# Kernel optimization log

Hardware: AMD Instinct MI355X
Metric: run time of the kernel (lower is better)

Reference implementation:

```python
import math
import jax, jax.numpy as jnp
import numpy as np

MIN_SIGMA = 1.0
MAX_SIGMA = 10.0
SIGMA_BINS = 50
TRUNCATE = 5.0
THRESHOLD = 0.001
H = W = 1024


def _make_sigmas():
    # np.linspace(min, max + (max-min)/bins, bins+1)
    return np.linspace(MIN_SIGMA, MAX_SIGMA + (MAX_SIGMA - MIN_SIGMA) / SIGMA_BINS,
                       num=SIGMA_BINS + 1).astype(np.float32)


def _make_pyramid_weight(sigmas):
    max_radius = int(TRUNCATE * float(sigmas.max()) + 0.5)
    size = 2 * max_radius + 1
    weight = np.zeros((len(sigmas), 1, size, size), dtype=np.float32)
    for i, s in enumerate(sigmas):
        r = int(TRUNCATE * float(s) + 0.5)
        ax = np.arange(2 * r + 1, dtype=np.float32)
        g = (1.0 / (s * math.sqrt(2 * math.pi))) * np.exp(-((ax - r) / s) ** 2 / 2)
        k = np.outer(g, g)
        k /= k.sum()
        pad = max_radius - r
        weight[i, 0, pad:pad + 2 * r + 1, pad:pad + 2 * r + 1] = k
    return weight, max_radius


def setup_inputs() -> dict:
    key = jax.random.key(0)
    sigmas_np = _make_sigmas()
    weight_np, _ = _make_pyramid_weight(sigmas_np)
    x = jax.random.normal(key, (1, 1, H, W), dtype=jnp.float32)
    return {
        "input": x,
        "weight": jnp.asarray(weight_np),            # [51, 1, 101, 101]
        "sigmas": jnp.asarray(sigmas_np),            # [51]
        "threshold": jnp.asarray(-THRESHOLD, dtype=jnp.float32),  # nn.Parameter(-threshold)
    }


def reference(input, weight, sigmas, threshold):
    max_radius = (weight.shape[-1] - 1) // 2
    # Gaussian pyramid: [1, 51, H, W], zero 'same' padding
    g = jax.lax.conv_general_dilated(
        input, weight,
        window_strides=(1, 1),
        padding=((max_radius, max_radius), (max_radius, max_radius)),
        dimension_numbers=("NCHW", "OIHW", "NCHW"),
    )[0]                                             # [51, H, W]
    # DoG scaled by sigma: [50, H, W]
    dog = (g[:-1] - g[1:]) * sigmas[:-1, None, None]
    # 3D local max pooling over (scale, y, x), kernel 3, stride 1, pad 1
    pooled = jax.lax.reduce_window(
        dog, -jnp.inf, jax.lax.max,
        window_dimensions=(3, 3, 3),
        window_strides=(1, 1, 1),
        padding=((1, 1), (1, 1), (1, 1)),
    )
    local_maxima = jax.nn.relu(pooled + threshold)
    soft_mask = 1.0 - (local_maxima - (dog + threshold))
    return local_maxima, soft_mask
```

## Files before the change

kernel.cpp:

```cpp
#include <hip/hip_runtime.h>
#include <cmath>

#define NS 51
#define ND 50
#define PLANE 1048576
#define DOG_ELEMS (ND * PLANE)
#define WPSTRIDE 160

__global__ void dog_prep(const float* __restrict__ weight,
                         float* __restrict__ wp,
                         int* __restrict__ rarr, int S) {
    int i = blockIdx.x;
    int t = threadIdx.x;
    int R = (S - 1) >> 1;
    const float* row = weight + ((size_t)i * S + R) * S;
    __shared__ float sr[128];
    __shared__ float ssum;
    __shared__ int spad;
    if (t < S) sr[t] = row[t];
    for (int j = t; j < WPSTRIDE; j += blockDim.x) wp[i * WPSTRIDE + j] = 0.f;
    __syncthreads();
    if (t == 0) {
        float sum = 0.f;
        for (int j = 0; j < S; ++j) sum += sr[j];
        int pad = 0;
        while (pad < R && sr[pad] == 0.f) ++pad;
        ssum = sum; spad = pad;
        rarr[i] = R - pad;
    }
    __syncthreads();
    int pad = spad;
    int r = R - pad;
    float inv = 1.f / ssum;
    for (int j = t; j <= 2 * r; j += blockDim.x)
        wp[i * WPSTRIDE + 17 + j] = sr[pad + j] * inv;
}

__global__ __launch_bounds__(256) void dog_hblur(
        const float* __restrict__ in, float* __restrict__ tmpH,
        const float* __restrict__ wp, const int* __restrict__ rarr) {
    const int lo_t[5] = {0, 17, 28, 37, 44};
    const int hi_t[5] = {17, 28, 37, 44, 51};
    int t = threadIdx.x;
    int grp = t >> 7;
    int tl = t & 127;
    int y = (blockIdx.x << 1) | grp;
    int zc = blockIdx.y;
    __shared__ float srow[2][1284];
    const float* inrow = in + ((size_t)y << 10);
    for (int f = tl; f < 286; f += 128) {
        int xg = (f << 2) - 56;
        float4 v = make_float4(0.f, 0.f, 0.f, 0.f);
        if (xg >= 0 && xg <= 1020) {
            v = *(const float4*)(inrow + xg);
        } else {
            float vv[4];
#pragma unroll
            for (int c = 0; c < 4; ++c) {
                int g = xg + c;
                vv[c] = ((unsigned)g < 1024u) ? inrow[g] : 0.f;
            }
            v = make_float4(vv[0], vv[1], vv[2], vv[3]);
        }
        int fs = f + (f >> 3);
        *(float4*)&srow[grp][fs << 2] = v;
    }
    __syncthreads();
    const float* s = srow[grp];
    for (int i = lo_t[zc]; i < hi_t[zc]; ++i) {
        int r = rarr[i];
        int c0 = 56 - r;
        int d = c0 & 7;
        int c0a = c0 - d;
        const float* __restrict__ w2 = wp + i * WPSTRIDE + 17 - d;
        int mcount = ((2 * r + d + 15) >> 3) << 3;
        float acc[8];
#pragma unroll
        for (int k = 0; k < 8; ++k) acc[k] = 0.f;
        int ft = (c0a >> 2) + (tl << 1);
        for (int m = 0; m < mcount; m += 8) {
            int f  = ft + (m >> 2);
            int fa = f + (f >> 3);
            int fb = (f + 1) + ((f + 1) >> 3);
            float4 va = *(const float4*)&s[fa << 2];
            float4 vb = *(const float4*)&s[fb << 2];
            float v[8] = {va.x, va.y, va.z, va.w, vb.x, vb.y, vb.z, vb.w};
#pragma unroll
            for (int j2 = 0; j2 < 8; ++j2)
#pragma unroll
                for (int k = 0; k < 8; ++k)
                    acc[k] = fmaf(w2[m + j2 - k], v[j2], acc[k]);
        }
        float* o = tmpH + (((size_t)i) << 20) + ((size_t)y << 10) + (tl << 3);
        *(float4*)o       = make_float4(acc[0], acc[1], acc[2], acc[3]);
        *(float4*)(o + 4) = make_float4(acc[4], acc[5], acc[6], acc[7]);
    }
}

#define FMAG(W, V, MM) do {                                                       \
_Pragma("unroll")                                                                 \
    for (int j_ = 0; j_ < 8; ++j_)                                                \
_Pragma("unroll")                                                                 \
        for (int k_ = 0; k_ < 10; ++k_)                                           \
            acc[k_] = fmaf((W)[17 + (MM) + j_ - k_], V[j_], acc[k_]);             \
    } while (0)

__global__ __launch_bounds__(512, 6) void dog_fused(
        const float* __restrict__ tmpH, float* __restrict__ out,
        const float* __restrict__ wp, const int* __restrict__ rarr,
        const float* __restrict__ sigmas, const float* __restrict__ thr_p) {
    const int jlo_t[5] = {0, 17, 28, 37, 44};
    const int jhi_t[5] = {16, 27, 36, 43, 49};
    int p = blockIdx.x;
    int xcd = p & 7;
    int q = p >> 3;
    int c8 = q >> 4;
    int ybg = q & 15;
    int combo = (c8 << 3) | xcd;
    if (combo >= 85) return;
    int wx = combo % 17;
    int zc = combo / 17;
    int t = threadIdx.x;
    int lane = t & 63;
    int wv = t >> 6;
    int y0u = __builtin_amdgcn_readfirstlane((ybg << 6) + (wv << 3));
    int x0 = wx * 62 - 1;
    int x = x0 + lane;
    int xa = x0 & ~3;
    int lx = (x0 - xa) + lane;
    bool xok = ((unsigned)x < 1024u);
    float thr = thr_p[0];
    const float NEG = -__builtin_huge_valf();

    __shared__ float stage[176 * 68];

    int jlo = jlo_t[zc], jhi = jhi_t[zc];
    int istart = jlo > 0 ? jlo - 1 : 0;
    int iend = (jhi + 2 < 50) ? jhi + 2 : 50;

    float gprev[10], A[8], B[8], Dprev[8];
#pragma unroll
    for (int k = 0; k < 10; ++k) gprev[k] = 0.f;
#pragma unroll
    for (int k = 0; k < 8; ++k) { A[k] = NEG; B[k] = NEG; Dprev[k] = 0.f; }

    for (int i = istart; i <= iend; ++i) {
        int r = rarr[i];
        const float* __restrict__ w = wp + i * WPSTRIDE;
        const float* __restrict__ plane = tmpH + ((size_t)i << 20);
        int mcount = ((2 * r + 17) >> 3) << 3;
        int nrows = mcount + 64;
        int gy0blk = (ybg << 6) - 1 - r;
        __syncthreads();
        int nf4 = nrows * 17;
        for (int e = t; e < nf4; e += 512) {
            int row = e / 17, c = e - row * 17;
            int gy = gy0blk + row;
            int gx = xa + (c << 2);
            float4 v = make_float4(0.f, 0.f, 0.f, 0.f);
            if ((unsigned)gy < 1024u) {
                const float* rp = plane + ((size_t)gy << 10);
                if ((unsigned)gx <= 1020u) {
                    v = *(const float4*)(rp + gx);
                } else {
                    float vv[4];
#pragma unroll
                    for (int cc = 0; cc < 4; ++cc) {
                        int g = gx + cc;
                        vv[cc] = ((unsigned)g < 1024u) ? rp[g] : 0.f;
                    }
                    v = make_float4(vv[0], vv[1], vv[2], vv[3]);
                }
            }
            *(float4*)(stage + row * 68 + (c << 2)) = v;
        }
        __syncthreads();
        float acc[10];
#pragma unroll
        for (int k = 0; k < 10; ++k) acc[k] = 0.f;
        int base = (wv << 3) * 68 + lx;
        for (int m = 0; m < mcount; m += 8) {
            float v[8];
#pragma unroll
            for (int j = 0; j < 8; ++j) v[j] = stage[base + (m + j) * 68];
            FMAG(w, v, m);
        }
        if (i > istart) {
            int d = i - 1;
            float sg = sigmas[d];
#pragma unroll
            for (int k = 0; k < 10; ++k) {
                int gy = y0u - 1 + k;
                bool ok = xok && ((unsigned)gy < 1024u);
                gprev[k] = ok ? (gprev[k] - acc[k]) * sg : NEG;
            }
            float ym[8];
#pragma unroll
            for (int k = 0; k < 8; ++k)
                ym[k] = fmaxf(fmaxf(gprev[k], gprev[k + 1]), gprev[k + 2]);
            if (d - 1 >= jlo) {
                float pooled[8];
#pragma unroll
                for (int k = 0; k < 8; ++k) {
                    float pn = fmaxf(B[k], ym[k]);
                    float l  = __shfl_up(pn, 1);
                    float rr = __shfl_down(pn, 1);
                    pooled[k] = fmaxf(fmaxf(l, rr), pn);
                }
                if (xok && lane >= 1 && lane <= 62) {
                    int j = d - 1;
#pragma unroll
                    for (int k = 0; k < 8; ++k) {
                        float lm = fmaxf(pooled[k] + thr, 0.f);
                        float sm = 1.f - lm + Dprev[k] + thr;
                        float* orow = out + (((size_t)j << 20)
                                     + ((size_t)(y0u + k) << 10));
                        __builtin_nontemporal_store(lm, orow + x);
                        __builtin_nontemporal_store(sm, orow + DOG_ELEMS + x);
                    }
                }
            }
#pragma unroll
            for (int k = 0; k < 8; ++k) {
                B[k] = fmaxf(A[k], ym[k]);
                A[k] = ym[k];
                Dprev[k] = gprev[k + 1];
            }
        }
#pragma unroll
        for (int k = 0; k < 10; ++k) gprev[k] = acc[k];
    }
    if (jhi == 49) {
        float pooled[8];
#pragma unroll
        for (int k = 0; k < 8; ++k) {
            float pn = B[k];
            float l  = __shfl_up(pn, 1);
            float rr = __shfl_down(pn, 1);
            pooled[k] = fmaxf(fmaxf(l, rr), pn);
        }
        if (xok && lane >= 1 && lane <= 62) {
#pragma unroll
            for (int k = 0; k < 8; ++k) {
                float lm = fmaxf(pooled[k] + thr, 0.f);
                float sm = 1.f - lm + Dprev[k] + thr;
                float* orow = out + (((size_t)49 << 20)
                             + ((size_t)(y0u + k) << 10));
                __builtin_nontemporal_store(lm, orow + x);
                __builtin_nontemporal_store(sm, orow + DOG_ELEMS + x);
            }
        }
    }
}

extern "C" void kernel_launch(void* const* d_in, const int* in_sizes, int n_in,
                              void* d_out, int out_size, void* d_ws, size_t ws_size,
                              hipStream_t stream) {
    const float* input  = (const float*)d_in[0];
    const float* weight = (const float*)d_in[1];
    const float* sigmas = (const float*)d_in[2];
    const float* thr    = (const float*)d_in[3];
    float* out = (float*)d_out;

    int S = 103;
    if (n_in > 1 && in_sizes[1] >= NS) {
        int s2 = in_sizes[1] / NS;
        S = (int)(sqrt((double)s2) + 0.5);
    }

    size_t need = ((size_t)NS * PLANE + NS * WPSTRIDE + 64) * 4 + 256;
    if (ws_size < need) return;

    float* tmpH = (float*)d_ws;
    float* wp   = tmpH + (size_t)NS * PLANE;
    int*   rarr = (int*)(wp + NS * WPSTRIDE);

    dog_prep <<<NS, 128, 0, stream>>>(weight, wp, rarr, S);
    dog_hblur<<<dim3(512, 5), 256, 0, stream>>>(input, tmpH, wp, rarr);
    dog_fused<<<1408, 512, 0, stream>>>(tmpH, out, wp, rarr, sigmas, thr);
}
```

Before: 379.4 us.

## Prefetch next scale plane into registers while computing current vertical convolution

The synchronous global-to-shared staging loop in the fused DoG kernel is replaced by a register double-buffer. Up to 6 float4 per thread (enough for the largest staged tile) are loaded for plane i+1 right after plane i is committed to shared memory. Those loads are then in flight while the vertical Gaussian FMAs run, hiding global-memory latency behind compute. The cost is 24 extra VGPRs per thread under tight launch bounds, which may reduce occupancy or cause spills.

New measurement: 737.6 us. 1.94x slower.

```diff
diff --git a/kernel.cpp b/kernel.cpp
--- a/kernel.cpp
+++ b/kernel.cpp
@@ -6,6 +6,7 @@
 #define PLANE 1048576
 #define DOG_ELEMS (ND * PLANE)
 #define WPSTRIDE 160
+#define NPF 6
 
 __global__ void dog_prep(const float* __restrict__ weight,
                          float* __restrict__ wp,
@@ -97,6 +98,7 @@
     }
 }
 
+
 #define FMAG(W, V, MM) do {                                                       \
 _Pragma("unroll")                                                                 \
     for (int j_ = 0; j_ < 8; ++j_)                                                \
@@ -104,6 +106,38 @@
         for (int k_ = 0; k_ < 10; ++k_)                                           \
             acc[k_] = fmaf((W)[17 + (MM) + j_ - k_], V[j_], acc[k_]);             \
     } while (0)
+
+#define PREF(ii) do {                                                             \
+    int r2_ = rarr[ii];                                                           \
+    const float* pl_ = tmpH + ((size_t)(ii) << 20);                               \
+    int mc2_ = ((2 * r2_ + 17) >> 3) << 3;                                        \
+    nf4c = (mc2_ + 64) * 17;                                                      \
+    int gyb_ = (ybg << 6) - 1 - r2_;                                              \
+_Pragma("unroll")                                                                 \
+    for (int k_ = 0; k_ < NPF; ++k_) {                                            \
+        int e_ = t + (k_ << 9);                                                   \
+        float4 v_ = make_float4(0.f, 0.f, 0.f, 0.f);                              \
+        if (e_ < nf4c) {                                                          \
+            int row_ = e_ / 17, c_ = e_ - row_ * 17;                              \
+            int gy_ = gyb_ + row_;                                                \
+            int gx_ = xa + (c_ << 2);                                             \
+            if ((unsigned)gy_ < 1024u) {                                          \
+                const float* rp_ = pl_ + ((size_t)gy_ << 10);                     \
+                if ((unsigned)gx_ <= 1020u) {                                     \
+                    v_ = *(const float4*)(rp_ + gx_);                             \
+                } else {                                                          \
+                    float vv_[4];                                                 \
+_Pragma("unroll")                                                                 \
+                    for (int cc_ = 0; cc_ < 4; ++cc_) {                           \
+                        int g_ = gx_ + cc_;                                       \
+                        vv_[cc_] = ((unsigned)g_ < 1024u) ? rp_[g_] : 0.f;        \
+                    }                                                             \
+                    v_ = make_float4(vv_[0], vv_[1], vv_[2], vv_[3]);             \
+                }                                                                 \
+            }                                                                     \
+        }                                                                         \
+        pv[k_] = v_;                                                              \
+    } } while (0)
 
 __global__ __launch_bounds__(512, 6) void dog_fused(
         const float* __restrict__ tmpH, float* __restrict__ out,
@@ -144,37 +178,26 @@
 #pragma unroll
     for (int k = 0; k < 8; ++k) { A[k] = NEG; B[k] = NEG; Dprev[k] = 0.f; }
 
+    float4 pv[NPF];
+    int nf4c;
+    PREF(istart);
+
     for (int i = istart; i <= iend; ++i) {
         int r = rarr[i];
         const float* __restrict__ w = wp + i * WPSTRIDE;
-        const float* __restrict__ plane = tmpH + ((size_t)i << 20);
         int mcount = ((2 * r + 17) >> 3) << 3;
-        int nrows = mcount + 64;
-        int gy0blk = (ybg << 6) - 1 - r;
         __syncthreads();
-        int nf4 = nrows * 17;
-        for (int e = t; e < nf4; e += 512) {
-            int row = e / 17, c = e - row * 17;
-            int gy = gy0blk + row;
-            int gx = xa + (c << 2);
-            float4 v = make_float4(0.f, 0.f, 0.f, 0.f);
-            if ((unsigned)gy < 1024u) {
-                const float* rp = plane + ((size_t)gy << 10);
-                if ((unsigned)gx <= 1020u) {
-                    v = *(const float4*)(rp + gx);
-                } else {
-                    float vv[4];
-#pragma unroll
-                    for (int cc = 0; cc < 4; ++cc) {
-                        int g = gx + cc;
-                        vv[cc] = ((unsigned)g < 1024u) ? rp[g] : 0.f;
-                    }
-                    v = make_float4(vv[0], vv[1], vv[2], vv[3]);
-                }
-            }
-            *(float4*)(stage + row * 68 + (c << 2)) = v;
+        int nf4 = nf4c;
+#pragma unroll
+        for (int k = 0; k < NPF; ++k) {
+            int e = t + (k << 9);
+            if (e < nf4) {
+                int row = e / 17, c = e - row * 17;
+                *(float4*)(stage + row * 68 + (c << 2)) = pv[k];
+            }
         }
         __syncthreads();
+        if (i < iend) PREF(i + 1);
         float acc[10];
 #pragma unroll
         for (int k = 0; k < 10; ++k) acc[k] = 0.f;
```

## Register-prefetch next scale plane tile while computing current vertical convolution

Applied to the files above, without the earlier changes.

Replaces the synchronous global-to-shared staging loop with a register double-buffer. The next plane's tile is loaded into six float4 registers per thread before the current plane's FMA loop runs, then written to shared memory at the start of the next iteration. This hides global load latency behind compute. In exchange it adds 24 live registers under launch_bounds(512,6), which risks spills or lower occupancy. It also grows the shared stage array so that fixed six-slot stores stay in bounds.

Measured after the change: 629.5 us. 65.9% more time.

```diff
diff --git a/kernel.cpp b/kernel.cpp
--- a/kernel.cpp
+++ b/kernel.cpp
@@ -97,6 +97,7 @@
     }
 }
 
+
 #define FMAG(W, V, MM) do {                                                       \
 _Pragma("unroll")                                                                 \
     for (int j_ = 0; j_ < 8; ++j_)                                                \
@@ -104,6 +105,46 @@
         for (int k_ = 0; k_ < 10; ++k_)                                           \
             acc[k_] = fmaf((W)[17 + (MM) + j_ - k_], V[j_], acc[k_]);             \
     } while (0)
+
+#define PREF1(PV, KK) do {                                                        \
+    int e_ = t + ((KK) << 9);                                                     \
+    int ec_ = e_ < nf4c ? e_ : nf4c - 1;                                          \
+    int row_ = ec_ / 17, c_ = ec_ - row_ * 17;                                    \
+    int gy_ = gyb + row_;                                                         \
+    int gx_ = xa + (c_ << 2);                                                     \
+    float4 v_ = make_float4(0.f, 0.f, 0.f, 0.f);                                  \
+    if ((unsigned)gy_ < 1024u) {                                                  \
+        const float* rp_ = plc + ((size_t)gy_ << 10);                             \
+        if ((unsigned)gx_ <= 1020u) {                                             \
+            v_ = *(const float4*)(rp_ + gx_);                                     \
+        } else {                                                                  \
+            float vv_[4];                                                         \
+_Pragma("unroll")                                                                 \
+            for (int cc_ = 0; cc_ < 4; ++cc_) {                                   \
+                int g_ = gx_ + cc_;                                               \
+                vv_[cc_] = ((unsigned)g_ < 1024u) ? rp_[g_] : 0.f;                \
+            }                                                                     \
+            v_ = make_float4(vv_[0], vv_[1], vv_[2], vv_[3]);                     \
+        }                                                                         \
+    }                                                                             \
+    PV = v_;                                                                      \
+} while (0)
+
+#define PREF(ii) do {                                                             \
+    int r2_ = rarr[ii];                                                           \
+    plc = tmpH + ((size_t)(ii) << 20);                                            \
+    int mc2_ = ((2 * r2_ + 17) >> 3) << 3;                                        \
+    nf4c = (mc2_ + 64) * 17;                                                      \
+    gyb = (ybg << 6) - 1 - r2_;                                                   \
+    PREF1(pv0, 0); PREF1(pv1, 1); PREF1(pv2, 2);                                  \
+    PREF1(pv3, 3); PREF1(pv4, 4); PREF1(pv5, 5);                                  \
+} while (0)
+
+#define STOREPV(PV, KK) do {                                                      \
+    int e_ = t + ((KK) << 9);                                                     \
+    int row_ = e_ / 17, c_ = e_ - row_ * 17;                                      \
+    *(float4*)(stage + row_ * 68 + (c_ << 2)) = PV;                               \
+} while (0)
 
 __global__ __launch_bounds__(512, 6) void dog_fused(
         const float* __restrict__ tmpH, float* __restrict__ out,
@@ -132,7 +173,7 @@
     float thr = thr_p[0];
     const float NEG = -__builtin_huge_valf();
 
-    __shared__ float stage[176 * 68];
+    __shared__ float stage[181 * 68];
 
     int jlo = jlo_t[zc], jhi = jhi_t[zc];
     int istart = jlo > 0 ? jlo - 1 : 0;
@@ -144,37 +185,20 @@
 #pragma unroll
     for (int k = 0; k < 8; ++k) { A[k] = NEG; B[k] = NEG; Dprev[k] = 0.f; }
 
+    float4 pv0, pv1, pv2, pv3, pv4, pv5;
+    const float* plc;
+    int nf4c, gyb;
+    PREF(istart);
+
     for (int i = istart; i <= iend; ++i) {
         int r = rarr[i];
         const float* __restrict__ w = wp + i * WPSTRIDE;
-        const float* __restrict__ plane = tmpH + ((size_t)i << 20);
         int mcount = ((2 * r + 17) >> 3) << 3;
-        int nrows = mcount + 64;
-        int gy0blk = (ybg << 6) - 1 - r;
         __syncthreads();
-        int nf4 = nrows * 17;
-        for (int e = t; e < nf4; e += 512) {
-            int row = e / 17, c = e - row * 17;
-            int gy = gy0blk + row;
-            int gx = xa + (c << 2);
-            float4 v = make_float4(0.f, 0.f, 0.f, 0.f);
-            if ((unsigned)gy < 1024u) {
-                const float* rp = plane + ((size_t)gy << 10);
-                if ((unsigned)gx <= 1020u) {
-                    v = *(const float4*)(rp + gx);
-                } else {
-                    float vv[4];
-#pragma unroll
-                    for (int cc = 0; cc < 4; ++cc) {
-                        int g = gx + cc;
-                        vv[cc] = ((unsigned)g < 1024u) ? rp[g] : 0.f;
-                    }
-                    v = make_float4(vv[0], vv[1], vv[2], vv[3]);
-                }
-            }
-            *(float4*)(stage + row * 68 + (c << 2)) = v;
-        }
+        STOREPV(pv0, 0); STOREPV(pv1, 1); STOREPV(pv2, 2);
+        STOREPV(pv3, 3); STOREPV(pv4, 4); STOREPV(pv5, 5);
         __syncthreads();
+        if (i < iend) PREF(i + 1);
         float acc[10];
 #pragma unroll
         for (int k = 0; k < 10; ++k) acc[k] = 0.f;
```
